# Kernel optimization log

Hardware: AMD Instinct MI355X
Metric: run time of the kernel (lower is better)

The kernel has to match this reference:

```python
import jax, jax.numpy as jnp
import numpy as np

N, E, ND, ED, H, L = 50000, 800000, 6, 4, 128, 4


def _ln(x, g, b, eps=1e-5):
    m = x.mean(-1, keepdims=True)
    v = ((x - m) ** 2).mean(-1, keepdims=True)
    return (x - m) * jax.lax.rsqrt(v + eps) * g + b


def _block(x, w1, b1, g1, be1, w2, b2, g2, be2):
    # Linear -> LayerNorm -> GELU -> (Dropout=identity in eval) -> Linear -> LayerNorm -> GELU
    h = jax.nn.gelu(_ln(x @ w1 + b1, g1, be1), approximate=False)
    return jax.nn.gelu(_ln(h @ w2 + b2, g2, be2), approximate=False)


def setup_inputs() -> dict:
    key = jax.random.key(0)
    ks = iter(jax.random.split(key, 16))
    w = lambda *s: jax.random.normal(next(ks), s, jnp.float32) * 0.05
    z = lambda *s: jnp.zeros(s, jnp.float32)
    o = lambda *s: jnp.ones(s, jnp.float32)
    return {
        "x": jax.random.normal(next(ks), (N, ND), jnp.float32),
        "edge_index": jax.random.randint(next(ks), (2, E), 0, N),
        "edge_attr": jax.random.normal(next(ks), (E, ED), jnp.float32),
        "ne_w1": w(ND, H), "ne_b1": z(H), "ne_g1": o(H), "ne_be1": z(H),
        "ne_w2": w(H, H), "ne_b2": z(H), "ne_g2": o(H), "ne_be2": z(H),
        "ee_w1": w(ED, H), "ee_b1": z(H), "ee_g1": o(H), "ee_be1": z(H),
        "ee_w2": w(H, H), "ee_b2": z(H), "ee_g2": o(H), "ee_be2": z(H),
        "cv_w1": w(L, H, H), "cv_b1": z(L, H), "cv_g1": o(L, H), "cv_be1": z(L, H),
        "cv_w2": w(L, H, H), "cv_b2": z(L, H), "cv_g2": o(L, H), "cv_be2": z(L, H),
        "nm_g": o(L, H), "nm_b": z(L, H),
        "dh_w1": w(H, H // 2), "dh_b1": z(H // 2), "dh_g": o(H // 2), "dh_be": z(H // 2),
        "dh_w2": w(H // 2, 3), "dh_b2": z(3),
        "sh_w1": w(H, H // 2), "sh_b1": z(H // 2), "sh_g": o(H // 2), "sh_be": z(H // 2),
        "sh_w2": w(H // 2, 1), "sh_b2": z(1),
    }


def reference(x, edge_index, edge_attr,
              ne_w1, ne_b1, ne_g1, ne_be1, ne_w2, ne_b2, ne_g2, ne_be2,
              ee_w1, ee_b1, ee_g1, ee_be1, ee_w2, ee_b2, ee_g2, ee_be2,
              cv_w1, cv_b1, cv_g1, cv_be1, cv_w2, cv_b2, cv_g2, cv_be2,
              nm_g, nm_b,
              dh_w1, dh_b1, dh_g, dh_be, dh_w2, dh_b2,
              sh_w1, sh_b1, sh_g, sh_be, sh_w2, sh_b2):
    h = _block(x, ne_w1, ne_b1, ne_g1, ne_be1, ne_w2, ne_b2, ne_g2, ne_be2)           # [N, H]
    e = _block(edge_attr, ee_w1, ee_b1, ee_g1, ee_be1, ee_w2, ee_b2, ee_g2, ee_be2)   # [E, H]
    src, dst = edge_index[0], edge_index[1]
    for l in range(L):
        # GINEConv (eps=0): sum_j relu(x_j + e_ij), then MLP((1+eps)*x + aggr)
        msg = jax.nn.relu(h[src] + e)                         # [E, H] gather + edge add
        agg = jax.ops.segment_sum(msg, dst, num_segments=N)   # [N, H] scatter-add
        u = _block(h + agg, cv_w1[l], cv_b1[l], cv_g1[l], cv_be1[l],
                   cv_w2[l], cv_b2[l], cv_g2[l], cv_be2[l])
        h = h + jax.nn.gelu(_ln(u, nm_g[l], nm_b[l]), approximate=False)  # residual
    d = jax.nn.gelu(_ln(h @ dh_w1 + dh_b1, dh_g, dh_be), approximate=False)
    displacement = d @ dh_w2 + dh_b2                          # [N, 3]
    s = jax.nn.gelu(_ln(h @ sh_w1 + sh_b1, sh_g, sh_be), approximate=False)
    stress = jax.nn.softplus(s @ sh_w2 + sh_b2)               # [N, 1]
    return displacement, stress, h
```

## Files before the change

### kernel.cpp

```cpp
#include <hip/hip_runtime.h>
#include <hip/hip_bf16.h>
#include <hip/hip_fp16.h>

#define HD 128
#define TILE 64
#define ST 136

typedef __attribute__((ext_vector_type(8))) short bf16x8;
typedef __attribute__((ext_vector_type(4))) float f32x4;

__device__ __forceinline__ float gelu_f(float x) {
    float y = fabsf(x) * 0.70710678118654752f;
    float t = __builtin_amdgcn_rcpf(fmaf(0.3275911f, y, 1.0f));
    float p = t * fmaf(t, fmaf(t, fmaf(t, fmaf(t, 1.061405429f, -1.453152027f),
                                       1.421413741f), -0.284496736f), 0.254829592f);
    float E = fmaf(-p, __expf(-y * y), 1.0f);
    return 0.5f * x * (1.0f + copysignf(E, x));
}
__device__ __forceinline__ unsigned short f2bf(float f) {
    unsigned int x = __float_as_uint(f);
    x = x + 0x7fffu + ((x >> 16) & 1u);
    return (unsigned short)(x >> 16);
}
__device__ __forceinline__ unsigned int pk2bf(float lo, float hi) {
    return (unsigned int)f2bf(lo) | ((unsigned int)f2bf(hi) << 16);
}
__device__ __forceinline__ float bf2f(unsigned short u) {
    return __uint_as_float((unsigned int)u << 16);
}
__device__ __forceinline__ unsigned int pk2h(float lo, float hi) {
    return (unsigned int)__half_as_ushort(__float2half(lo)) |
           ((unsigned int)__half_as_ushort(__float2half(hi)) << 16);
}
__device__ __forceinline__ float h2f_lo(unsigned int u) {
    return __half2float(__ushort_as_half((unsigned short)(u & 0xffffu)));
}
__device__ __forceinline__ float h2f_hi(unsigned int u) {
    return __half2float(__ushort_as_half((unsigned short)(u >> 16)));
}

__device__ __forceinline__ void mm_mfma(const unsigned short* sA, int wrow, int lane,
                                        const unsigned short* __restrict__ wt, f32x4 acc[8]) {
    int m = lane & 15, kb = lane >> 4;
    bf16x8 a[4];
#pragma unroll
    for (int kk = 0; kk < 4; ++kk)
        a[kk] = *(const bf16x8*)(sA + (wrow + m) * ST + kk * 32 + kb * 8);
#pragma unroll
    for (int n0 = 0; n0 < 8; ++n0) {
        f32x4 c = {0.f, 0.f, 0.f, 0.f};
#pragma unroll
        for (int kk = 0; kk < 4; ++kk) {
            bf16x8 b = *(const bf16x8*)(wt + ((size_t)((n0 * 4 + kk) * 64 + lane)) * 8);
            c = __builtin_amdgcn_mfma_f32_16x16x32_bf16(b, a[kk], c, 0, 0, 0);
        }
        acc[n0] = c;
    }
}

__device__ __forceinline__ void mm_mfma2(const unsigned short* sH, const unsigned short* sL,
                                         int wrow, int lane,
                                         const unsigned short* __restrict__ wt, f32x4 acc[8]) {
    int m = lane & 15, kb = lane >> 4;
    bf16x8 ah[4], al[4];
#pragma unroll
    for (int kk = 0; kk < 4; ++kk) {
        ah[kk] = *(const bf16x8*)(sH + (wrow + m) * ST + kk * 32 + kb * 8);
        al[kk] = *(const bf16x8*)(sL + (wrow + m) * ST + kk * 32 + kb * 8);
    }
#pragma unroll
    for (int n0 = 0; n0 < 8; ++n0) {
        f32x4 c = {0.f, 0.f, 0.f, 0.f};
#pragma unroll
        for (int kk = 0; kk < 4; ++kk) {
            bf16x8 b = *(const bf16x8*)(wt + ((size_t)((n0 * 4 + kk) * 64 + lane)) * 8);
            c = __builtin_amdgcn_mfma_f32_16x16x32_bf16(b, ah[kk], c, 0, 0, 0);
            c = __builtin_amdgcn_mfma_f32_16x16x32_bf16(b, al[kk], c, 0, 0, 0);
        }
        acc[n0] = c;
    }
}

__device__ __forceinline__ void bias_ln_gelu(f32x4 acc[8], float u[8][4],
                                             const float* bias, const float* g,
                                             const float* be, int kb) {
    float s = 0.f, ss = 0.f;
#pragma unroll
    for (int n0 = 0; n0 < 8; ++n0)
#pragma unroll
        for (int q = 0; q < 4; ++q) {
            float x = acc[n0][q] + bias[n0 * 16 + kb * 4 + q];
            u[n0][q] = x;
            s += x; ss += x * x;
        }
    s += __shfl_xor(s, 16); ss += __shfl_xor(ss, 16);
    s += __shfl_xor(s, 32); ss += __shfl_xor(ss, 32);
    float mean = s * (1.f / HD);
    float inv = rsqrtf(ss * (1.f / HD) - mean * mean + 1e-5f);
#pragma unroll
    for (int n0 = 0; n0 < 8; ++n0)
#pragma unroll
        for (int q = 0; q < 4; ++q) {
            int c = n0 * 16 + kb * 4 + q;
            u[n0][q] = gelu_f((u[n0][q] - mean) * inv * g[c] + be[c]);
        }
}

__global__ void prep_weights(const float* __restrict__ ne_w2, const float* __restrict__ ee_w2,
                             const float* __restrict__ cv_w1, const float* __restrict__ cv_w2,
                             unsigned short* __restrict__ wbf) {
    int mat = blockIdx.x;
    const float* src = (mat == 0) ? ne_w2
                     : (mat == 1) ? ee_w2
                     : (mat < 6)  ? cv_w1 + (size_t)(mat - 2) * HD * HD
                                  : cv_w2 + (size_t)(mat - 6) * HD * HD;
    unsigned short* dst = wbf + (size_t)mat * HD * HD;
    for (int i = threadIdx.x; i < HD * HD; i += 256) {
        int e = i & 7, lane = (i >> 3) & 63, f = i >> 9;
        int m = lane & 15, kb = lane >> 4;
        int n0 = f >> 2, kk = f & 3;
        int k = kk * 32 + kb * 8 + e;
        int c = n0 * 16 + m;
        dst[i] = f2bf(src[(size_t)k * HD + c]);
    }
}

template <int IN_DIM, bool EDGE>
__global__ __launch_bounds__(256) void encoder_mfma(
    const float* __restrict__ in, const float* __restrict__ w1,
    const float* __restrict__ b1, const float* __restrict__ g1,
    const float* __restrict__ be1, const unsigned short* __restrict__ wt2,
    const float* __restrict__ b2, const float* __restrict__ g2,
    const float* __restrict__ be2, float* __restrict__ h_out,
    unsigned short* __restrict__ e_perm, const int* __restrict__ pos, int rows) {
    __shared__ __align__(16) unsigned short s_A[TILE * ST];
    __shared__ float s_vec[6][HD];
    __shared__ int s_pos[TILE];

    int tid = threadIdx.x;
    int row0 = blockIdx.x * TILE;
    if (tid < HD) {
        s_vec[0][tid] = b1[tid]; s_vec[1][tid] = g1[tid]; s_vec[2][tid] = be1[tid];
        s_vec[3][tid] = b2[tid]; s_vec[4][tid] = g2[tid]; s_vec[5][tid] = be2[tid];
    }
    if (EDGE && tid < TILE) {
        int gr = row0 + tid;
        s_pos[tid] = (gr < rows) ? pos[gr] : 0;
    }
    __syncthreads();

    int tr = tid >> 4, tc = tid & 15;
    int r0 = tr * 4, c0 = tc * 8;
    float w1r[IN_DIM][8];
#pragma unroll
    for (int k = 0; k < IN_DIM; ++k) {
        float4 pa = *(const float4*)(w1 + (size_t)k * HD + c0);
        float4 pb = *(const float4*)(w1 + (size_t)k * HD + c0 + 4);
        w1r[k][0] = pa.x; w1r[k][1] = pa.y; w1r[k][2] = pa.z; w1r[k][3] = pa.w;
        w1r[k][4] = pb.x; w1r[k][5] = pb.y; w1r[k][6] = pb.z; w1r[k][7] = pb.w;
    }
    float v[4][8];
#pragma unroll
    for (int i = 0; i < 4; ++i)
#pragma unroll
        for (int j = 0; j < 8; ++j) v[i][j] = s_vec[0][c0 + j];
#pragma unroll
    for (int i = 0; i < 4; ++i) {
        int gr = min(row0 + r0 + i, rows - 1);
        float xr[IN_DIM];
        if constexpr (IN_DIM == 4) {
            float4 t4 = *(const float4*)(in + (size_t)gr * 4);
            xr[0] = t4.x; xr[1] = t4.y; xr[2] = t4.z; xr[3] = t4.w;
        } else {
#pragma unroll
            for (int k = 0; k < IN_DIM; ++k) xr[k] = in[(size_t)gr * IN_DIM + k];
        }
#pragma unroll
        for (int k = 0; k < IN_DIM; ++k)
#pragma unroll
            for (int j = 0; j < 8; ++j) v[i][j] = fmaf(xr[k], w1r[k][j], v[i][j]);
    }
#pragma unroll
    for (int i = 0; i < 4; ++i) {
        float s = 0.f, ss = 0.f;
#pragma unroll
        for (int j = 0; j < 8; ++j) { s += v[i][j]; ss += v[i][j] * v[i][j]; }
#pragma unroll
        for (int msk = 1; msk < 16; msk <<= 1) { s += __shfl_xor(s, msk); ss += __shfl_xor(ss, msk); }
        float mean = s * (1.f / HD);
        float inv = rsqrtf(ss * (1.f / HD) - mean * mean + 1e-5f);
#pragma unroll
        for (int j = 0; j < 8; ++j)
            v[i][j] = gelu_f((v[i][j] - mean) * inv * s_vec[1][c0 + j] + s_vec[2][c0 + j]);
        uint4 q4;
        q4.x = pk2bf(v[i][0], v[i][1]); q4.y = pk2bf(v[i][2], v[i][3]);
        q4.z = pk2bf(v[i][4], v[i][5]); q4.w = pk2bf(v[i][6], v[i][7]);
        *(uint4*)&s_A[(r0 + i) * ST + c0] = q4;
    }
    __syncthreads();

    int wave = tid >> 6, lane = tid & 63;
    int m = lane & 15, kb = lane >> 4;
    int wrow = wave * 16;
    f32x4 acc[8];
    mm_mfma(s_A, wrow, lane, wt2, acc);
    float u[8][4];
    bias_ln_gelu(acc, u, s_vec[3], s_vec[4], s_vec[5], kb);

    if (EDGE) {
        __syncthreads();
#pragma unroll
        for (int n0 = 0; n0 < 8; ++n0) {
            uint2 p;
            p.x = pk2h(u[n0][0], u[n0][1]);
            p.y = pk2h(u[n0][2], u[n0][3]);
            *(uint2*)&s_A[(wrow + m) * ST + n0 * 16 + kb * 4] = p;
        }
        __syncthreads();
#pragma unroll
        for (int i = 0; i < 4; ++i) {
            int c = tid + i * 256;
            int r = c >> 4, cc = (c & 15) * 8;
            int gr = row0 + r;
            if (gr < rows) {
                uint4 q4 = *(uint4*)&s_A[r * ST + cc];
                *(uint4*)(e_perm + (size_t)s_pos[r] * HD + cc) = q4;
            }
        }
    } else {
        int grow = row0 + wrow + m;
        if (grow < rows) {
#pragma unroll
            for (int n0 = 0; n0 < 8; ++n0)
                *(float4*)(h_out + (size_t)grow * HD + n0 * 16 + kb * 4) =
                    make_float4(u[n0][0], u[n0][1], u[n0][2], u[n0][3]);
        }
    }
}

__global__ __launch_bounds__(256) void conv_mfma(
    const unsigned short* __restrict__ tin_hi, const unsigned short* __restrict__ tin_lo,
    float* __restrict__ h,
    const unsigned short* __restrict__ wt1, const float* __restrict__ b1,
    const float* __restrict__ g1, const float* __restrict__ be1,
    const unsigned short* __restrict__ wt2, const float* __restrict__ b2,
    const float* __restrict__ g2, const float* __restrict__ be2,
    const float* __restrict__ nmg, const float* __restrict__ nmb, int rows) {
    __shared__ __align__(16) unsigned short s_A[TILE * ST];
    __shared__ __align__(16) unsigned short s_L[TILE * ST];
    __shared__ float s_vec[8][HD];

    int tid = threadIdx.x;
    int row0 = blockIdx.x * TILE;
    if (tid < HD) {
        s_vec[0][tid] = b1[tid];  s_vec[1][tid] = g1[tid];  s_vec[2][tid] = be1[tid];
        s_vec[3][tid] = b2[tid];  s_vec[4][tid] = g2[tid];  s_vec[5][tid] = be2[tid];
        s_vec[6][tid] = nmg[tid]; s_vec[7][tid] = nmb[tid];
    }
#pragma unroll
    for (int i = 0; i < 4; ++i) {
        int c = tid + i * 256;
        int r = c >> 4, cc = (c & 15) * 8;
        int gr = min(row0 + r, rows - 1);
        *(uint4*)&s_A[r * ST + cc] = *(const uint4*)(tin_hi + (size_t)gr * HD + cc);
        *(uint4*)&s_L[r * ST + cc] = *(const uint4*)(tin_lo + (size_t)gr * HD + cc);
    }
    __syncthreads();

    int wave = tid >> 6, lane = tid & 63;
    int m = lane & 15, kb = lane >> 4;
    int wrow = wave * 16;
    f32x4 acc[8];
    float u[8][4];

    mm_mfma2(s_A, s_L, wrow, lane, wt1, acc);
    bias_ln_gelu(acc, u, s_vec[0], s_vec[1], s_vec[2], kb);
    __syncthreads();
#pragma unroll
    for (int n0 = 0; n0 < 8; ++n0) {
        uint2 p;
        p.x = pk2bf(u[n0][0], u[n0][1]);
        p.y = pk2bf(u[n0][2], u[n0][3]);
        *(uint2*)&s_A[(wrow + m) * ST + n0 * 16 + kb * 4] = p;
    }
    __syncthreads();

    mm_mfma(s_A, wrow, lane, wt2, acc);
    bias_ln_gelu(acc, u, s_vec[3], s_vec[4], s_vec[5], kb);
    {
        float s = 0.f, ss = 0.f;
#pragma unroll
        for (int n0 = 0; n0 < 8; ++n0)
#pragma unroll
            for (int q = 0; q < 4; ++q) { s += u[n0][q]; ss += u[n0][q] * u[n0][q]; }
        s += __shfl_xor(s, 16); ss += __shfl_xor(ss, 16);
        s += __shfl_xor(s, 32); ss += __shfl_xor(ss, 32);
        float mean = s * (1.f / HD);
        float inv = rsqrtf(ss * (1.f / HD) - mean * mean + 1e-5f);
#pragma unroll
        for (int n0 = 0; n0 < 8; ++n0)
#pragma unroll
            for (int q = 0; q < 4; ++q) {
                int c = n0 * 16 + kb * 4 + q;
                u[n0][q] = gelu_f((u[n0][q] - mean) * inv * s_vec[6][c] + s_vec[7][c]);
            }
    }
    int grow = row0 + wrow + m;
    if (grow < rows) {
#pragma unroll
        for (int n0 = 0; n0 < 8; ++n0) {
            size_t idx = (size_t)grow * HD + n0 * 16 + kb * 4;
            float4 hv = *(const float4*)(h + idx);
            hv.x += u[n0][0]; hv.y += u[n0][1]; hv.z += u[n0][2]; hv.w += u[n0][3];
            *(float4*)(h + idx) = hv;
        }
    }
}

__global__ void zero_kernel(int* p, int n) {
    int i = blockIdx.x * 256 + threadIdx.x;
    if (i < n) p[i] = 0;
}
__global__ void hist_kernel(const int* __restrict__ dst, int* __restrict__ cnt, int n) {
    for (int i = blockIdx.x * 256 + threadIdx.x; i < n; i += gridDim.x * 256)
        atomicAdd(&cnt[dst[i]], 1);
}
__global__ __launch_bounds__(1024) void scan_block_kernel(
    const int* __restrict__ cnt, int* __restrict__ incl, int* __restrict__ bsum, int n) {
    __shared__ int buf[2][1024];
    int t = threadIdx.x;
    int i = blockIdx.x * 1024 + t;
    int v = (i < n) ? cnt[i] : 0;
    buf[0][t] = v;
    __syncthreads();
    int pin = 0;
    for (int off = 1; off < 1024; off <<= 1) {
        int x = buf[pin][t];
        if (t >= off) x += buf[pin][t - off];
        buf[pin ^ 1][t] = x;
        __syncthreads();
        pin ^= 1;
    }
    if (i < n) incl[i] = buf[pin][t];
    if (t == 1023) bsum[blockIdx.x] = buf[pin][t];
}
__global__ void scan_top_kernel(int* bsum, int nb) {
    int t = threadIdx.x;
    int v = (t < nb) ? bsum[t] : 0;
    int orig = v;
#pragma unroll
    for (int off = 1; off < 64; off <<= 1) {
        int y = __shfl_up(v, off);
        if (t >= off) v += y;
    }
    if (t < nb) bsum[t] = v - orig;
}
__global__ void add_off_kernel(int* __restrict__ offs, const int* __restrict__ bsum,
                               int* __restrict__ cursor, int n) {
    int i = blockIdx.x * 256 + threadIdx.x;
    if (i == 0) { offs[0] = 0; cursor[0] = 0; }
    if (i < n) {
        int v = offs[i + 1] + bsum[i >> 10];
        offs[i + 1] = v;
        if (i + 1 < n) cursor[i + 1] = v;
    }
}
__global__ void scatter_kernel(const int* __restrict__ dstArr, int* __restrict__ cursor,
                               int* __restrict__ eidslot, int n) {
    for (int i = blockIdx.x * 256 + threadIdx.x; i < n; i += gridDim.x * 256) {
        int d = dstArr[i];
        int p = atomicAdd(&cursor[d], 1);
        eidslot[p] = i;
    }
}
__global__ void sort_seg_kernel(const int* __restrict__ offs, int* __restrict__ eidslot, int n) {
    int node = blockIdx.x * 256 + threadIdx.x;
    if (node >= n) return;
    int beg = offs[node], end = offs[node + 1];
    for (int p = beg + 1; p < end; ++p) {
        int v = eidslot[p];
        int q = p - 1;
        while (q >= beg && eidslot[q] > v) { eidslot[q + 1] = eidslot[q]; --q; }
        eidslot[q + 1] = v;
    }
}
__global__ void finalize_kernel(const int* __restrict__ srcArr, int* __restrict__ eidslot,
                                int* __restrict__ pos, int n) {
    int p = blockIdx.x * 256 + threadIdx.x;
    if (p < n) {
        int t = eidslot[p];
        pos[t] = p;
        eidslot[p] = srcArr[t];
    }
}

__global__ __launch_bounds__(256) void aggregate_kernel(
    const float* __restrict__ h, const unsigned short* __restrict__ e,
    const int* __restrict__ offs, const int* __restrict__ esrc,
    unsigned short* __restrict__ tin_hi, unsigned short* __restrict__ tin_lo, int nnodes) {
    int wave = threadIdx.x >> 6, lane = threadIdx.x & 63;
    int n = blockIdx.x * 4 + wave;
    if (n >= nnodes) return;
    int beg = offs[n], end = offs[n + 1];
    float ax = 0.f, ay = 0.f;
    int i = beg;
    for (; i + 4 <= end; i += 4) {
        int s0 = esrc[i], s1 = esrc[i + 1], s2 = esrc[i + 2], s3 = esrc[i + 3];
        float2 h0 = *(const float2*)(h + (size_t)s0 * HD + 2 * lane);
        float2 h1 = *(const float2*)(h + (size_t)s1 * HD + 2 * lane);
        float2 h2 = *(const float2*)(h + (size_t)s2 * HD + 2 * lane);
        float2 h3 = *(const float2*)(h + (size_t)s3 * HD + 2 * lane);
        unsigned int e0 = *(const unsigned int*)(e + (size_t)(i + 0) * HD + 2 * lane);
        unsigned int e1 = *(const unsigned int*)(e + (size_t)(i + 1) * HD + 2 * lane);
        unsigned int e2 = *(const unsigned int*)(e + (size_t)(i + 2) * HD + 2 * lane);
        unsigned int e3 = *(const unsigned int*)(e + (size_t)(i + 3) * HD + 2 * lane);
        ax += fmaxf(h0.x + h2f_lo(e0), 0.f);
        ay += fmaxf(h0.y + h2f_hi(e0), 0.f);
        ax += fmaxf(h1.x + h2f_lo(e1), 0.f);
        ay += fmaxf(h1.y + h2f_hi(e1), 0.f);
        ax += fmaxf(h2.x + h2f_lo(e2), 0.f);
        ay += fmaxf(h2.y + h2f_hi(e2), 0.f);
        ax += fmaxf(h3.x + h2f_lo(e3), 0.f);
        ay += fmaxf(h3.y + h2f_hi(e3), 0.f);
    }
    for (; i < end; ++i) {
        int src = esrc[i];
        float2 hv = *(const float2*)(h + (size_t)src * HD + 2 * lane);
        unsigned int ue = *(const unsigned int*)(e + (size_t)i * HD + 2 * lane);
        ax += fmaxf(hv.x + h2f_lo(ue), 0.f);
        ay += fmaxf(hv.y + h2f_hi(ue), 0.f);
    }
    float2 hn = *(const float2*)(h + (size_t)n * HD + 2 * lane);
    float tx = hn.x + ax, ty = hn.y + ay;
    unsigned short hx = f2bf(tx), hy = f2bf(ty);
    float lx = tx - bf2f(hx), ly = ty - bf2f(hy);
    *(unsigned int*)(tin_hi + (size_t)n * HD + 2 * lane) =
        (unsigned int)hx | ((unsigned int)hy << 16);
    *(unsigned int*)(tin_lo + (size_t)n * HD + 2 * lane) = pk2bf(lx, ly);
}

__global__ __launch_bounds__(256) void head_kernel(
    const float* __restrict__ h, const float* __restrict__ dw1,
    const float* __restrict__ db1, const float* __restrict__ dg,
    const float* __restrict__ dbe, const float* __restrict__ dw2,
    const float* __restrict__ db2, const float* __restrict__ sw1,
    const float* __restrict__ sb1, const float* __restrict__ sg,
    const float* __restrict__ sbe, const float* __restrict__ sw2,
    const float* __restrict__ sb2, float* __restrict__ out, int nnodes) {
    __shared__ float s_wd[HD * 64];
    __shared__ float s_ws[HD * 64];
    __shared__ float s_vd[3][64];
    __shared__ float s_vs[3][64];
    __shared__ float s_w2d[64 * 3];
    __shared__ float s_w2s[64];
    __shared__ float s_h[4][HD];
    __shared__ float s_b2[4];

    int tid = threadIdx.x;
    for (int i = tid; i < HD * 64; i += 256) { s_wd[i] = dw1[i]; s_ws[i] = sw1[i]; }
    if (tid < 64) {
        s_vd[0][tid] = db1[tid]; s_vd[1][tid] = dg[tid]; s_vd[2][tid] = dbe[tid];
        s_vs[0][tid] = sb1[tid]; s_vs[1][tid] = sg[tid]; s_vs[2][tid] = sbe[tid];
        s_w2s[tid] = sw2[tid];
    }
    if (tid < 64 * 3) s_w2d[tid] = dw2[tid];
    if (tid == 0) { s_b2[0] = db2[0]; s_b2[1] = db2[1]; s_b2[2] = db2[2]; s_b2[3] = sb2[0]; }
    __syncthreads();

    int wave = tid >> 6, lane = tid & 63;
    float* disp = out;
    float* stress = out + (size_t)nnodes * 3;
    float* hout = out + (size_t)nnodes * 4;

    for (int n = blockIdx.x * 4 + wave; n < nnodes; n += gridDim.x * 4) {
        float2 hv = *(const float2*)(h + (size_t)n * HD + lane * 2);
        *(float2*)(hout + (size_t)n * HD + lane * 2) = hv;
        s_h[wave][lane * 2] = hv.x;
        s_h[wave][lane * 2 + 1] = hv.y;
        float accd = s_vd[0][lane], accs = s_vs[0][lane];
        for (int k = 0; k < HD; ++k) {
            float hx = s_h[wave][k];
            accd = fmaf(hx, s_wd[k * 64 + lane], accd);
            accs = fmaf(hx, s_ws[k * 64 + lane], accs);
        }
        float s = accd, ss = accd * accd;
#pragma unroll
        for (int msk = 1; msk < 64; msk <<= 1) { s += __shfl_xor(s, msk); ss += __shfl_xor(ss, msk); }
        float mean = s * (1.f / 64), inv = rsqrtf(ss * (1.f / 64) - mean * mean + 1e-5f);
        float d = gelu_f((accd - mean) * inv * s_vd[1][lane] + s_vd[2][lane]);
        s = accs; ss = accs * accs;
#pragma unroll
        for (int msk = 1; msk < 64; msk <<= 1) { s += __shfl_xor(s, msk); ss += __shfl_xor(ss, msk); }
        mean = s * (1.f / 64); inv = rsqrtf(ss * (1.f / 64) - mean * mean + 1e-5f);
        float sv = gelu_f((accs - mean) * inv * s_vs[1][lane] + s_vs[2][lane]);
        float p0 = d * s_w2d[lane * 3 + 0];
        float p1 = d * s_w2d[lane * 3 + 1];
        float p2 = d * s_w2d[lane * 3 + 2];
        float ps = sv * s_w2s[lane];
#pragma unroll
        for (int msk = 1; msk < 64; msk <<= 1) {
            p0 += __shfl_xor(p0, msk); p1 += __shfl_xor(p1, msk);
            p2 += __shfl_xor(p2, msk); ps += __shfl_xor(ps, msk);
        }
        if (lane == 0) {
            disp[(size_t)n * 3 + 0] = p0 + s_b2[0];
            disp[(size_t)n * 3 + 1] = p1 + s_b2[1];
            disp[(size_t)n * 3 + 2] = p2 + s_b2[2];
            float xs = ps + s_b2[3];
            stress[n] = fmaxf(xs, 0.f) + log1pf(expf(-fabsf(xs)));
        }
    }
}

extern "C" void kernel_launch(void* const* d_in, const int* in_sizes, int n_in,
                              void* d_out, int out_size, void* d_ws, size_t ws_size,
                              hipStream_t stream) {
    const float* x = (const float*)d_in[0];
    const int* ei = (const int*)d_in[1];
    const float* ea = (const float*)d_in[2];
    const float* ne_w1 = (const float*)d_in[3];
    const float* ne_b1 = (const float*)d_in[4];
    const float* ne_g1 = (const float*)d_in[5];
    const float* ne_be1 = (const float*)d_in[6];
    const float* ne_w2 = (const float*)d_in[7];
    const float* ne_b2 = (const float*)d_in[8];
    const float* ne_g2 = (const float*)d_in[9];
    const float* ne_be2 = (const float*)d_in[10];
    const float* ee_w1 = (const float*)d_in[11];
    const float* ee_b1 = (const float*)d_in[12];
    const float* ee_g1 = (const float*)d_in[13];
    const float* ee_be1 = (const float*)d_in[14];
    const float* ee_w2 = (const float*)d_in[15];
    const float* ee_b2 = (const float*)d_in[16];
    const float* ee_g2 = (const float*)d_in[17];
    const float* ee_be2 = (const float*)d_in[18];
    const float* cv_w1 = (const float*)d_in[19];
    const float* cv_b1 = (const float*)d_in[20];
    const float* cv_g1 = (const float*)d_in[21];
    const float* cv_be1 = (const float*)d_in[22];
    const float* cv_w2 = (const float*)d_in[23];
    const float* cv_b2 = (const float*)d_in[24];
    const float* cv_g2 = (const float*)d_in[25];
    const float* cv_be2 = (const float*)d_in[26];
    const float* nm_g = (const float*)d_in[27];
    const float* nm_b = (const float*)d_in[28];
    const float* dh_w1 = (const float*)d_in[29];
    const float* dh_b1 = (const float*)d_in[30];
    const float* dh_g = (const float*)d_in[31];
    const float* dh_be = (const float*)d_in[32];
    const float* dh_w2 = (const float*)d_in[33];
    const float* dh_b2 = (const float*)d_in[34];
    const float* sh_w1 = (const float*)d_in[35];
    const float* sh_b1 = (const float*)d_in[36];
    const float* sh_g = (const float*)d_in[37];
    const float* sh_be = (const float*)d_in[38];
    const float* sh_w2 = (const float*)d_in[39];
    const float* sh_b2 = (const float*)d_in[40];

    int N = in_sizes[0] / 6;
    int E = in_sizes[1] / 2;

    char* wp = (char*)d_ws;
    auto take = [&](size_t bytes) {
        char* p = wp;
        wp += (bytes + 255) & ~(size_t)255;
        return p;
    };
    unsigned short* e_perm = (unsigned short*)take((size_t)E * HD * 2);
    float* h = (float*)take((size_t)N * HD * 4);
    unsigned short* tin_hi = (unsigned short*)take((size_t)N * HD * 2);
    unsigned short* tin_lo = (unsigned short*)take((size_t)N * HD * 2);
    unsigned short* wbf = (unsigned short*)take((size_t)10 * HD * HD * 2);
    int* cnt = (int*)take((size_t)N * 4);
    int* offs = (int*)take((size_t)(N + 1) * 4);
    int* cursor = (int*)take((size_t)N * 4);
    int* bsum = (int*)take(256);
    int* pos = (int*)take((size_t)E * 4);
    int* esrc = (int*)take((size_t)E * 4);

    const int* srcArr = ei;
    const int* dstArr = ei + E;

    int nbN = (N + TILE - 1) / TILE;
    int nbE = (E + TILE - 1) / TILE;

    prep_weights<<<10, 256, 0, stream>>>(ne_w2, ee_w2, cv_w1, cv_w2, wbf);
    zero_kernel<<<(N + 255) / 256, 256, 0, stream>>>(cnt, N);
    hist_kernel<<<2048, 256, 0, stream>>>(dstArr, cnt, E);
    int nsb = (N + 1023) / 1024;
    scan_block_kernel<<<nsb, 1024, 0, stream>>>(cnt, offs + 1, bsum, N);
    scan_top_kernel<<<1, 64, 0, stream>>>(bsum, nsb);
    add_off_kernel<<<(N + 255) / 256, 256, 0, stream>>>(offs, bsum, cursor, N);
    scatter_kernel<<<2048, 256, 0, stream>>>(dstArr, cursor, esrc, E);
    sort_seg_kernel<<<(N + 255) / 256, 256, 0, stream>>>(offs, esrc, N);
    finalize_kernel<<<(E + 255) / 256, 256, 0, stream>>>(srcArr, esrc, pos, E);

    encoder_mfma<6, false><<<nbN, 256, 0, stream>>>(
        x, ne_w1, ne_b1, ne_g1, ne_be1, wbf + 0 * HD * HD, ne_b2, ne_g2, ne_be2,
        h, nullptr, nullptr, N);
    encoder_mfma<4, true><<<nbE, 256, 0, stream>>>(
        ea, ee_w1, ee_b1, ee_g1, ee_be1, wbf + 1 * HD * HD, ee_b2, ee_g2, ee_be2,
        nullptr, e_perm, pos, E);

    for (int l = 0; l < 4; ++l) {
        aggregate_kernel<<<(N + 3) / 4, 256, 0, stream>>>(h, e_perm, offs, esrc,
                                                          tin_hi, tin_lo, N);
        conv_mfma<<<nbN, 256, 0, stream>>>(
            tin_hi, tin_lo, h, wbf + (size_t)(2 + l) * HD * HD, cv_b1 + l * HD,
            cv_g1 + l * HD, cv_be1 + l * HD, wbf + (size_t)(6 + l) * HD * HD,
            cv_b2 + l * HD, cv_g2 + l * HD, cv_be2 + l * HD,
            nm_g + l * HD, nm_b + l * HD, N);
    }

    head_kernel<<<1024, 256, 0, stream>>>(h, dh_w1, dh_b1, dh_g, dh_be, dh_w2, dh_b2,
                                          sh_w1, sh_b1, sh_g, sh_be, sh_w2, sh_b2,
                                          (float*)d_out, N);
}
```

Before: 941.2 us.

## Store node features as split fp16 hi/lo planes to halve gather traffic

Node features h are now kept in two fp16 arrays (a high part and a low residual) in place of one fp32 array. The edge aggregation gathers only the high fp16 part for each neighbour, which halves the bytes read per gathered edge. The self term, the residual update and the head still rebuild near-fp32 values from both parts. The cost is lower precision in the neighbour messages and some extra conversion work in the conv and head kernels.

Result: faster. 859.6 us (-8.7%).

```diff
diff --git a/kernel.cpp b/kernel.cpp
--- a/kernel.cpp
+++ b/kernel.cpp
@@ -37,6 +37,11 @@
 }
 __device__ __forceinline__ float h2f_hi(unsigned int u) {
     return __half2float(__ushort_as_half((unsigned short)(u >> 16)));
+}
+__device__ __forceinline__ void split_h(float v, unsigned short& hi, unsigned short& lo) {
+    __half hh = __float2half(v);
+    hi = __half_as_ushort(hh);
+    lo = __half_as_ushort(__float2half(v - __half2float(hh)));
 }
 
 __device__ __forceinline__ void mm_mfma(const unsigned short* sA, int wrow, int lane,
@@ -131,8 +136,9 @@
     const float* __restrict__ b1, const float* __restrict__ g1,
     const float* __restrict__ be1, const unsigned short* __restrict__ wt2,
     const float* __restrict__ b2, const float* __restrict__ g2,
-    const float* __restrict__ be2, float* __restrict__ h_out,
-    unsigned short* __restrict__ e_perm, const int* __restrict__ pos, int rows) {
+    const float* __restrict__ be2, unsigned short* __restrict__ h_hi,
+    unsigned short* __restrict__ h_lo, unsigned short* __restrict__ e_perm,
+    const int* __restrict__ pos, int rows) {
     __shared__ __align__(16) unsigned short s_A[TILE * ST];
     __shared__ float s_vec[6][HD];
     __shared__ int s_pos[TILE];
@@ -231,16 +237,26 @@
         int grow = row0 + wrow + m;
         if (grow < rows) {
 #pragma unroll
-            for (int n0 = 0; n0 < 8; ++n0)
-                *(float4*)(h_out + (size_t)grow * HD + n0 * 16 + kb * 4) =
-                    make_float4(u[n0][0], u[n0][1], u[n0][2], u[n0][3]);
+            for (int n0 = 0; n0 < 8; ++n0) {
+                size_t idx = (size_t)grow * HD + n0 * 16 + kb * 4;
+                unsigned short hi0, lo0, hi1, lo1, hi2, lo2, hi3, lo3;
+                split_h(u[n0][0], hi0, lo0); split_h(u[n0][1], hi1, lo1);
+                split_h(u[n0][2], hi2, lo2); split_h(u[n0][3], hi3, lo3);
+                uint2 ph, pl;
+                ph.x = (unsigned int)hi0 | ((unsigned int)hi1 << 16);
+                ph.y = (unsigned int)hi2 | ((unsigned int)hi3 << 16);
+                pl.x = (unsigned int)lo0 | ((unsigned int)lo1 << 16);
+                pl.y = (unsigned int)lo2 | ((unsigned int)lo3 << 16);
+                *(uint2*)(h_hi + idx) = ph;
+                *(uint2*)(h_lo + idx) = pl;
+            }
         }
     }
 }
 
 __global__ __launch_bounds__(256) void conv_mfma(
     const unsigned short* __restrict__ tin_hi, const unsigned short* __restrict__ tin_lo,
-    float* __restrict__ h,
+    unsigned short* __restrict__ h_hi, unsigned short* __restrict__ h_lo,
     const unsigned short* __restrict__ wt1, const float* __restrict__ b1,
     const float* __restrict__ g1, const float* __restrict__ be1,
     const unsigned short* __restrict__ wt2, const float* __restrict__ b2,
@@ -310,9 +326,21 @@
 #pragma unroll
         for (int n0 = 0; n0 < 8; ++n0) {
             size_t idx = (size_t)grow * HD + n0 * 16 + kb * 4;
-            float4 hv = *(const float4*)(h + idx);
-            hv.x += u[n0][0]; hv.y += u[n0][1]; hv.z += u[n0][2]; hv.w += u[n0][3];
-            *(float4*)(h + idx) = hv;
+            uint2 ph = *(const uint2*)(h_hi + idx);
+            uint2 pl = *(const uint2*)(h_lo + idx);
+            float v0 = h2f_lo(ph.x) + h2f_lo(pl.x) + u[n0][0];
+            float v1 = h2f_hi(ph.x) + h2f_hi(pl.x) + u[n0][1];
+            float v2 = h2f_lo(ph.y) + h2f_lo(pl.y) + u[n0][2];
+            float v3 = h2f_hi(ph.y) + h2f_hi(pl.y) + u[n0][3];
+            unsigned short hi0, lo0, hi1, lo1, hi2, lo2, hi3, lo3;
+            split_h(v0, hi0, lo0); split_h(v1, hi1, lo1);
+            split_h(v2, hi2, lo2); split_h(v3, hi3, lo3);
+            ph.x = (unsigned int)hi0 | ((unsigned int)hi1 << 16);
+            ph.y = (unsigned int)hi2 | ((unsigned int)hi3 << 16);
+            pl.x = (unsigned int)lo0 | ((unsigned int)lo1 << 16);
+            pl.y = (unsigned int)lo2 | ((unsigned int)lo3 << 16);
+            *(uint2*)(h_hi + idx) = ph;
+            *(uint2*)(h_lo + idx) = pl;
         }
     }
 }
@@ -395,7 +423,8 @@
 }
 
 __global__ __launch_bounds__(256) void aggregate_kernel(
-    const float* __restrict__ h, const unsigned short* __restrict__ e,
+    const unsigned short* __restrict__ h_hi, const unsigned short* __restrict__ h_lo,
+    const unsigned short* __restrict__ e,
     const int* __restrict__ offs, const int* __restrict__ esrc,
     unsigned short* __restrict__ tin_hi, unsigned short* __restrict__ tin_lo, int nnodes) {
     int wave = threadIdx.x >> 6, lane = threadIdx.x & 63;
@@ -406,32 +435,34 @@
     int i = beg;
     for (; i + 4 <= end; i += 4) {
         int s0 = esrc[i], s1 = esrc[i + 1], s2 = esrc[i + 2], s3 = esrc[i + 3];
-        float2 h0 = *(const float2*)(h + (size_t)s0 * HD + 2 * lane);
-        float2 h1 = *(const float2*)(h + (size_t)s1 * HD + 2 * lane);
-        float2 h2 = *(const float2*)(h + (size_t)s2 * HD + 2 * lane);
-        float2 h3 = *(const float2*)(h + (size_t)s3 * HD + 2 * lane);
+        unsigned int g0 = *(const unsigned int*)(h_hi + (size_t)s0 * HD + 2 * lane);
+        unsigned int g1 = *(const unsigned int*)(h_hi + (size_t)s1 * HD + 2 * lane);
+        unsigned int g2 = *(const unsigned int*)(h_hi + (size_t)s2 * HD + 2 * lane);
+        unsigned int g3 = *(const unsigned int*)(h_hi + (size_t)s3 * HD + 2 * lane);
         unsigned int e0 = *(const unsigned int*)(e + (size_t)(i + 0) * HD + 2 * lane);
         unsigned int e1 = *(const unsigned int*)(e + (size_t)(i + 1) * HD + 2 * lane);
         unsigned int e2 = *(const unsigned int*)(e + (size_t)(i + 2) * HD + 2 * lane);
         unsigned int e3 = *(const unsigned int*)(e + (size_t)(i + 3) * HD + 2 * lane);
-        ax += fmaxf(h0.x + h2f_lo(e0), 0.f);
-        ay += fmaxf(h0.y + h2f_hi(e0), 0.f);
-        ax += fmaxf(h1.x + h2f_lo(e1), 0.f);
-        ay += fmaxf(h1.y + h2f_hi(e1), 0.f);
-        ax += fmaxf(h2.x + h2f_lo(e2), 0.f);
-        ay += fmaxf(h2.y + h2f_hi(e2), 0.f);
-        ax += fmaxf(h3.x + h2f_lo(e3), 0.f);
-        ay += fmaxf(h3.y + h2f_hi(e3), 0.f);
+        ax += fmaxf(h2f_lo(g0) + h2f_lo(e0), 0.f);
+        ay += fmaxf(h2f_hi(g0) + h2f_hi(e0), 0.f);
+        ax += fmaxf(h2f_lo(g1) + h2f_lo(e1), 0.f);
+        ay += fmaxf(h2f_hi(g1) + h2f_hi(e1), 0.f);
+        ax += fmaxf(h2f_lo(g2) + h2f_lo(e2), 0.f);
+        ay += fmaxf(h2f_hi(g2) + h2f_hi(e2), 0.f);
+        ax += fmaxf(h2f_lo(g3) + h2f_lo(e3), 0.f);
+        ay += fmaxf(h2f_hi(g3) + h2f_hi(e3), 0.f);
     }
     for (; i < end; ++i) {
         int src = esrc[i];
-        float2 hv = *(const float2*)(h + (size_t)src * HD + 2 * lane);
+        unsigned int gh = *(const unsigned int*)(h_hi + (size_t)src * HD + 2 * lane);
         unsigned int ue = *(const unsigned int*)(e + (size_t)i * HD + 2 * lane);
-        ax += fmaxf(hv.x + h2f_lo(ue), 0.f);
-        ay += fmaxf(hv.y + h2f_hi(ue), 0.f);
-    }
-    float2 hn = *(const float2*)(h + (size_t)n * HD + 2 * lane);
-    float tx = hn.x + ax, ty = hn.y + ay;
+        ax += fmaxf(h2f_lo(gh) + h2f_lo(ue), 0.f);
+        ay += fmaxf(h2f_hi(gh) + h2f_hi(ue), 0.f);
+    }
+    unsigned int shh = *(const unsigned int*)(h_hi + (size_t)n * HD + 2 * lane);
+    unsigned int shl = *(const unsigned int*)(h_lo + (size_t)n * HD + 2 * lane);
+    float tx = (h2f_lo(shh) + h2f_lo(shl)) + ax;
+    float ty = (h2f_hi(shh) + h2f_hi(shl)) + ay;
     unsigned short hx = f2bf(tx), hy = f2bf(ty);
     float lx = tx - bf2f(hx), ly = ty - bf2f(hy);
     *(unsigned int*)(tin_hi + (size_t)n * HD + 2 * lane) =
@@ -440,7 +471,8 @@
 }
 
 __global__ __launch_bounds__(256) void head_kernel(
-    const float* __restrict__ h, const float* __restrict__ dw1,
+    const unsigned short* __restrict__ h_hi, const unsigned short* __restrict__ h_lo,
+    const float* __restrict__ dw1,
     const float* __restrict__ db1, const float* __restrict__ dg,
     const float* __restrict__ dbe, const float* __restrict__ dw2,
     const float* __restrict__ db2, const float* __restrict__ sw1,
@@ -473,10 +505,13 @@
     float* hout = out + (size_t)nnodes * 4;
 
     for (int n = blockIdx.x * 4 + wave; n < nnodes; n += gridDim.x * 4) {
-        float2 hv = *(const float2*)(h + (size_t)n * HD + lane * 2);
-        *(float2*)(hout + (size_t)n * HD + lane * 2) = hv;
-        s_h[wave][lane * 2] = hv.x;
-        s_h[wave][lane * 2 + 1] = hv.y;
+        unsigned int ph = *(const unsigned int*)(h_hi + (size_t)n * HD + lane * 2);
+        unsigned int pl = *(const unsigned int*)(h_lo + (size_t)n * HD + lane * 2);
+        float hvx = h2f_lo(ph) + h2f_lo(pl);
+        float hvy = h2f_hi(ph) + h2f_hi(pl);
+        *(float2*)(hout + (size_t)n * HD + lane * 2) = make_float2(hvx, hvy);
+        s_h[wave][lane * 2] = hvx;
+        s_h[wave][lane * 2 + 1] = hvy;
         float accd = s_vd[0][lane], accs = s_vs[0][lane];
         for (int k = 0; k < HD; ++k) {
             float hx = s_h[wave][k];
@@ -567,7 +602,8 @@
         return p;
     };
     unsigned short* e_perm = (unsigned short*)take((size_t)E * HD * 2);
-    float* h = (float*)take((size_t)N * HD * 4);
+    unsigned short* h_hi = (unsigned short*)take((size_t)N * HD * 2);
+    unsigned short* h_lo = (unsigned short*)take((size_t)N * HD * 2);
     unsigned short* tin_hi = (unsigned short*)take((size_t)N * HD * 2);
     unsigned short* tin_lo = (unsigned short*)take((size_t)N * HD * 2);
     unsigned short* wbf = (unsigned short*)take((size_t)10 * HD * HD * 2);
@@ -597,22 +633,22 @@
 
     encoder_mfma<6, false><<<nbN, 256, 0, stream>>>(
         x, ne_w1, ne_b1, ne_g1, ne_be1, wbf + 0 * HD * HD, ne_b2, ne_g2, ne_be2,
-        h, nullptr, nullptr, N);
+        h_hi, h_lo, nullptr, nullptr, N);
     encoder_mfma<4, true><<<nbE, 256, 0, stream>>>(
         ea, ee_w1, ee_b1, ee_g1, ee_be1, wbf + 1 * HD * HD, ee_b2, ee_g2, ee_be2,
-        nullptr, e_perm, pos, E);
+        nullptr, nullptr, e_perm, pos, E);
 
     for (int l = 0; l < 4; ++l) {
-        aggregate_kernel<<<(N + 3) / 4, 256, 0, stream>>>(h, e_perm, offs, esrc,
+        aggregate_kernel<<<(N + 3) / 4, 256, 0, stream>>>(h_hi, h_lo, e_perm, offs, esrc,
                                                           tin_hi, tin_lo, N);
         conv_mfma<<<nbN, 256, 0, stream>>>(
-            tin_hi, tin_lo, h, wbf + (size_t)(2 + l) * HD * HD, cv_b1 + l * HD,
+            tin_hi, tin_lo, h_hi, h_lo, wbf + (size_t)(2 + l) * HD * HD, cv_b1 + l * HD,
             cv_g1 + l * HD, cv_be1 + l * HD, wbf + (size_t)(6 + l) * HD * HD,
             cv_b2 + l * HD, cv_g2 + l * HD, cv_be2 + l * HD,
             nm_g + l * HD, nm_b + l * HD, N);
     }
 
-    head_kernel<<<1024, 256, 0, stream>>>(h, dh_w1, dh_b1, dh_g, dh_be, dh_w2, dh_b2,
-                                          sh_w1, sh_b1, sh_g, sh_be, sh_w2, sh_b2,
-                                          (float*)d_out, N);
-}
+    head_kernel<<<1024, 256, 0, stream>>>(h_hi, h_lo, dh_w1, dh_b1, dh_g, dh_be,
+                                          dh_w2, dh_b2, sh_w1, sh_b1, sh_g, sh_be,
+                                          sh_w2, sh_b2, (float*)d_out, N);
+}
```
